# Kernel optimization log

Hardware: AMD Instinct MI355X
Metric: run time of the kernel (lower is better)

## Reference

```python
import jax, jax.numpy as jnp
import numpy as np

N_RBF = 20
CUTOFF = 5.0
N_BASIS = 128
N_FILTERS = 128
N_LAYERS = 3
B, N = 128, 128
N_PAIRS = 524288


def ssp(x):
    # ShiftedSoftplus: softplus(x) - log(2)
    return jax.nn.softplus(x) - jnp.log(2.0).astype(x.dtype)


def gaussian_rbf(d):
    # schnetpack-style GaussianRBF: offsets in [0, cutoff], shared width
    offsets = jnp.linspace(0.0, CUTOFF, N_RBF, dtype=d.dtype)
    width = offsets[1] - offsets[0]
    coeff = -0.5 / (width * width)
    diff = d[:, None] - offsets[None, :]  # [n_pairs, n_rbf]
    return jnp.exp(coeff * diff * diff)


def cosine_cutoff(d):
    fc = 0.5 * (jnp.cos(d * (jnp.pi / CUTOFF)) + 1.0)
    return fc * (d < CUTOFF).astype(d.dtype)


def setup_inputs() -> dict:
    key = jax.random.key(0)
    ks = jax.random.split(key, 16)
    inp = {
        "Z": jax.random.randint(ks[0], (B, N), 0, 100),
        "R": jax.random.normal(ks[1], (B, N, 3), dtype=jnp.float32) * 2.0,
        "idx_i": jax.random.randint(ks[2], (N_PAIRS,), 0, B * N),
        "idx_j": jax.random.randint(ks[3], (N_PAIRS,), 0, B * N),
        "emb": jax.random.normal(ks[4], (100, N_BASIS), dtype=jnp.float32) * 0.1,
    }
    s = 0.05
    inp["in2f_W"] = jax.random.normal(ks[5], (N_LAYERS, N_BASIS, N_FILTERS), dtype=jnp.float32) * s
    inp["in2f_b"] = jnp.zeros((N_LAYERS, N_FILTERS), dtype=jnp.float32)
    inp["fW1"] = jax.random.normal(ks[6], (N_LAYERS, N_RBF, N_FILTERS), dtype=jnp.float32) * s
    inp["fb1"] = jnp.zeros((N_LAYERS, N_FILTERS), dtype=jnp.float32)
    inp["fW2"] = jax.random.normal(ks[7], (N_LAYERS, N_FILTERS, N_FILTERS), dtype=jnp.float32) * s
    inp["fb2"] = jnp.zeros((N_LAYERS, N_FILTERS), dtype=jnp.float32)
    inp["oW1"] = jax.random.normal(ks[8], (N_LAYERS, N_FILTERS, N_BASIS), dtype=jnp.float32) * s
    inp["ob1"] = jnp.zeros((N_LAYERS, N_BASIS), dtype=jnp.float32)
    inp["oW2"] = jax.random.normal(ks[9], (N_LAYERS, N_BASIS, N_BASIS), dtype=jnp.float32) * s
    inp["ob2"] = jnp.zeros((N_LAYERS, N_BASIS), dtype=jnp.float32)
    return inp


def _interaction(x, f_ij, rcut_ij, idx_i, idx_j, W_in, b_in, fW1, fb1, fW2, fb2, oW1, ob1, oW2, ob2):
    # x: [B, N, n_atom_basis]
    h = jnp.einsum("bnf,fg->bng", x, W_in) + b_in          # input_to_feature
    h = h.reshape(-1, h.shape[-1])                           # [B*N, n_filters]
    # filter network on RBFs
    Wij = ssp(f_ij @ fW1 + fb1) @ fW2 + fb2                  # [n_pairs, n_filters]
    Wij = Wij * rcut_ij[:, None]
    x_ij = h[idx_j] * Wij                                     # gather + multiply
    agg = jax.ops.segment_sum(x_ij, idx_i, num_segments=h.shape[0])  # scatter_add
    out = ssp(agg @ oW1 + ob1) @ oW2 + ob2                    # feature_to_output
    return out.reshape(x.shape[0], x.shape[1], N_BASIS)


def reference(Z, R, idx_i, idx_j, emb, in2f_W, in2f_b, fW1, fb1, fW2, fb2, oW1, ob1, oW2, ob2):
    coords = R.reshape(-1, 3)                                 # [B*N, 3]
    vec = coords[idx_i] - coords[idx_j]
    d_ij = jnp.linalg.norm(vec, axis=-1)                      # [n_pairs]
    f_ij = gaussian_rbf(d_ij)                                 # [n_pairs, 20]
    rcut_ij = cosine_cutoff(d_ij)                             # [n_pairs]
    x = emb[Z]                                                # [B, N, 128]
    for l in range(N_LAYERS):
        v = _interaction(x, f_ij, rcut_ij, idx_i, idx_j,
                         in2f_W[l], in2f_b[l], fW1[l], fb1[l], fW2[l], fb2[l],
                         oW1[l], ob1[l], oW2[l], ob2[l])
        x = x + v
    return x
```

## Files before the change

### kernel.cpp

```cpp
#include <hip/hip_runtime.h>
#include <hip/hip_fp16.h>

#define NPAIRS 524288
#define NATOMS 16384
#define TBINS  2048
#define TROWS  2049
#define CAP    80
#define CUTOFF_F 5.0f

typedef _Float16 f16;
typedef f16 f16x4 __attribute__((ext_vector_type(4)));
typedef f16 f16x8 __attribute__((ext_vector_type(8)));
typedef float f32x4 __attribute__((ext_vector_type(4)));

__device__ __forceinline__ float sspf(float v) {
  float a = fabsf(v);
  return fmaxf(v, 0.0f) + log1pf(expf(-a)) - 0.69314718055994531f;
}

__device__ __forceinline__ int swz(int row, int kh) {
  return (row << 8) + ((kh << 1) ^ ((row & 7) << 4));
}
__device__ __forceinline__ int swzW(int col, int kh) {
  return (col << 7) + ((kh << 1) ^ ((col & 7) << 4));
}
__device__ __forceinline__ f16x8 ldW(const f16* __restrict__ Wg, int col, int ss, int hi) {
  return *(const f16x8*)((const char*)Wg + (ss >> 1) * 16384 + swzW(col, (ss & 1) * 32 + hi * 8));
}

__device__ __forceinline__ uint4 ldtab(const f16* __restrict__ tabL, int v, int c) {
  return *(const uint4*)(tabL + ((unsigned)(v >> 14) << 7) + (c << 3));
}
__device__ __forceinline__ uint4 ldh(const f16* __restrict__ hin, int v, int c) {
  return *(const uint4*)(hin + ((unsigned)(v & 16383) << 7) + (c << 3));
}
__device__ __forceinline__ void dot8(float* acc, uint4 wv, uint4 hv) {
  const __half* wp = (const __half*)&wv;
  const __half* hp = (const __half*)&hv;
  #pragma unroll
  for (int q = 0; q < 8; ++q)
    acc[q] = fmaf(__half2float(wp[q]), __half2float(hp[q]), acc[q]);
}

__global__ __launch_bounds__(256) void prep(const float* __restrict__ fW1,
                                            const float* __restrict__ fb1,
                                            const float* __restrict__ fW2,
                                            const float* __restrict__ fb2,
                                            f16* __restrict__ table,
                                            const float* __restrict__ in2f_W,
                                            const float* __restrict__ oW1,
                                            const float* __restrict__ oW2,
                                            f16* __restrict__ wsw,
                                            int* __restrict__ cursor) {
  __shared__ float hid[8 * 128];
  int t = threadIdx.x;
  int bid = blockIdx.x;

  if (bid >= 843) { cursor[(bid - 843) * 256 + t] = 0; return; }

  if (bid >= 771) {
    int bid2 = bid - 771;
    int mm = bid2 >> 3;
    int tloc = (bid2 & 7) * 256 + t;
    int col = tloc & 127, k0 = (tloc >> 7) << 3;
    const float* src = mm < 3 ? in2f_W + (size_t)mm * 16384
                     : mm < 6 ? oW1 + (size_t)(mm - 3) * 16384
                              : oW2 + (size_t)(mm - 6) * 16384;
    f16x8 v;
    #pragma unroll
    for (int kk = 0; kk < 8; ++kk) v[kk] = (f16)src[(k0 + kk) * 128 + col];
    *(f16x8*)((char*)wsw + (size_t)mm * 32768 + (k0 >> 6) * 16384 + swzW(col, k0 & 63)) = v;
    return;
  }

  int l = bid / 257, rem = bid % 257;
  int e = t >> 5, q = t & 31;
  int ti = rem * 8 + e;
  const float* W1 = fW1 + (size_t)l * 20 * 128;
  const float* B1 = fb1 + (size_t)l * 128;
  const float* W2 = fW2 + (size_t)l * 128 * 128;
  const float* B2 = fb2 + (size_t)l * 128;

  const float width = CUTOFF_F / 19.0f;
  const float coeff = -0.5f / (width * width);
  const float dstep = CUTOFF_F / (float)TBINS;
  float d = (float)ti * dstep;

  float4 h4 = *(const float4*)&B1[q * 4];
  #pragma unroll
  for (int r = 0; r < 20; ++r) {
    float diff = d - (float)r * width;
    float fr = expf(coeff * diff * diff);
    float4 w4 = *(const float4*)&W1[r * 128 + q * 4];
    h4.x += fr * w4.x; h4.y += fr * w4.y; h4.z += fr * w4.z; h4.w += fr * w4.w;
  }
  *(float4*)&hid[e * 128 + q * 4] =
      make_float4(sspf(h4.x), sspf(h4.y), sspf(h4.z), sspf(h4.w));
  __syncthreads();

  float4 o4 = *(const float4*)&B2[q * 4];
  const float4* W2g = (const float4*)W2;
  #pragma unroll 4
  for (int g = 0; g < 128; ++g) {
    float hv = hid[e * 128 + g];
    float4 w4 = W2g[g * 32 + q];
    o4.x += hv * w4.x; o4.y += hv * w4.y; o4.z += hv * w4.z; o4.w += hv * w4.w;
  }

  if (ti < TROWS) {
    float fc = (d < CUTOFF_F) ? 0.5f * (cosf(d * 0.62831853071795865f) + 1.0f) : 0.0f;
    f16x4 hv = { (f16)(o4.x * fc), (f16)(o4.y * fc), (f16)(o4.z * fc), (f16)(o4.w * fc) };
    *(f16x4*)((f16*)table + ((size_t)l * TROWS + ti) * 128 + q * 4) = hv;
  }
}

__global__ __launch_bounds__(256) void pg0(const int* __restrict__ Z,
                                           const float* __restrict__ emb,
                                           const f16* __restrict__ Wsw,
                                           const float* __restrict__ bias,
                                           f16* __restrict__ hout,
                                           const int* __restrict__ idx_i,
                                           const int* __restrict__ idx_j,
                                           const float* __restrict__ R,
                                           int* __restrict__ cursor,
                                           int* __restrict__ pjd) {
  int t = threadIdx.x;

  if (blockIdx.x < 2048) {
    int p = blockIdx.x * 256 + t;
    int i = idx_i[p], j = idx_j[p];
    float dx = R[(size_t)i*3+0] - R[(size_t)j*3+0];
    float dy = R[(size_t)i*3+1] - R[(size_t)j*3+1];
    float dz = R[(size_t)i*3+2] - R[(size_t)j*3+2];
    float d = sqrtf(dx*dx + dy*dy + dz*dz);
    if (d < CUTOFF_F) {
      int bin = __float2int_rn(d * ((float)TBINS / CUTOFF_F));
      int slot = atomicAdd(&cursor[i], 1);
      if (slot < CAP) pjd[i * CAP + slot] = j | (bin << 14);
    }
    return;
  }

  size_t rbase = (size_t)(blockIdx.x - 2048) * 64;
  int w = t >> 6, lane = t & 63;
  int lo = lane & 15, hi = lane >> 4;

  int z = Z[rbase + 16 * w + lo];
  const float* erow = emb + (size_t)z * 128;
  f16x8 fa[4];
  #pragma unroll
  for (int ss = 0; ss < 4; ++ss) {
    float4 a = *(const float4*)(erow + ss * 32 + hi * 8);
    float4 b = *(const float4*)(erow + ss * 32 + hi * 8 + 4);
    f16x8 v = { (f16)a.x, (f16)a.y, (f16)a.z, (f16)a.w,
                (f16)b.x, (f16)b.y, (f16)b.z, (f16)b.w };
    fa[ss] = v;
  }

  #pragma unroll
  for (int cb = 0; cb < 8; ++cb) {
    int col = cb * 16 + lo;
    f32x4 acc = {0.0f, 0.0f, 0.0f, 0.0f};
    #pragma unroll
    for (int ss = 0; ss < 4; ++ss)
      acc = __builtin_amdgcn_mfma_f32_16x16x32_f16(fa[ss], ldW(Wsw, col, ss, hi), acc, 0, 0, 0);
    float bc = bias[col];
    #pragma unroll
    for (int j = 0; j < 4; ++j)
      hout[(rbase + 16 * w + hi * 4 + j) * 128 + col] = (f16)(acc[j] + bc);
  }
}

template <int FIRST, int HAS_NEXT>
__global__ __launch_bounds__(1024, 8) void aggfuse(const int* __restrict__ pjd,
                                                   const int* __restrict__ cnt,
                                                   const f16* __restrict__ hin,
                                                   const f16* __restrict__ tabL,
                                                   const f16* __restrict__ W1g,
                                                   const float* __restrict__ ob1,
                                                   const f16* __restrict__ W2g,
                                                   const float* __restrict__ ob2,
                                                   const int* __restrict__ Z,
                                                   const float* __restrict__ emb,
                                                   float* __restrict__ x,
                                                   const f16* __restrict__ Wng,
                                                   const float* __restrict__ bn,
                                                   f16* __restrict__ hout) {
  __shared__ char smem[16384];
  char* AlT = smem;
  char* Tl  = smem + 8192;
  int tid = threadIdx.x;
  int wv = tid >> 6, lane = tid & 63;
  int s = lane >> 4, c = lane & 15;
  int rbase = blockIdx.x * 32;
  const int S = (TBINS << 14);

  {
    int a = rbase + wv * 2 + (s & 1);
    int half = s >> 1;
    int p0 = a * CAP;
    int n = min(cnt[a], CAP);
    int nh = half * 2;

    int m = (n + 3) >> 2;
    m = max(m, __shfl_xor(m, 16, 64));
    m = max(m, __shfl_xor(m, 32, 64));

    float acc[8];
    #pragma unroll
    for (int q = 0; q < 8; ++q) acc[q] = 0.0f;

    int vA  = (nh < n)     ? pjd[p0 + nh]     : S;
    int vB  = (nh + 1 < n) ? pjd[p0 + nh + 1] : S;
    int vA1 = (nh + 4 < n) ? pjd[p0 + nh + 4] : S;
    int vB1 = (nh + 5 < n) ? pjd[p0 + nh + 5] : S;
    uint4 wA = ldtab(tabL, vA, c), hA = ldh(hin, vA, c);
    uint4 wB = ldtab(tabL, vB, c), hB = ldh(hin, vB, c);

    for (int it = 0; it < m; ++it) {
      int k2 = 4 * (it + 2) + nh;
      int vA2 = (k2 < n)     ? pjd[p0 + k2]     : S;
      int vB2 = (k2 + 1 < n) ? pjd[p0 + k2 + 1] : S;
      uint4 wAn = ldtab(tabL, vA1, c), hAn = ldh(hin, vA1, c);
      uint4 wBn = ldtab(tabL, vB1, c), hBn = ldh(hin, vB1, c);
      dot8(acc, wA, hA);
      dot8(acc, wB, hB);
      wA = wAn; hA = hAn; wB = wBn; hB = hBn;
      vA1 = vA2; vB1 = vB2;
    }

    #pragma unroll
    for (int q = 0; q < 8; ++q) acc[q] += __shfl_xor(acc[q], 32, 64);

    if (s < 2) {
      int row = wv * 2 + s;
      f16x8 pk;
      #pragma unroll
      for (int q = 0; q < 8; ++q) pk[q] = (f16)acc[q];
      *(f16x8*)(AlT + swz(row, c * 8)) = pk;
    }
  }
  __syncthreads();

  int lo = c, hi = s;
  int col = (wv & 7) * 16 + lo;
  int rb16 = (wv >> 3) * 16;

  float res[4];
  if (FIRST) {
    #pragma unroll
    for (int j = 0; j < 4; ++j) {
      int z = Z[rbase + rb16 + hi * 4 + j];
      res[j] = emb[(size_t)z * 128 + col];
    }
  } else {
    #pragma unroll
    for (int j = 0; j < 4; ++j)
      res[j] = x[(size_t)(rbase + rb16 + hi * 4 + j) * 128 + col];
  }

  {
    f32x4 acc = {0.0f, 0.0f, 0.0f, 0.0f};
    #pragma unroll
    for (int ss = 0; ss < 4; ++ss) {
      f16x8 fa = *(f16x8*)(AlT + swz(rb16 + lo, ss * 32 + hi * 8));
      acc = __builtin_amdgcn_mfma_f32_16x16x32_f16(fa, ldW(W1g, col, ss, hi), acc, 0, 0, 0);
    }
    float bc = ob1[col];
    #pragma unroll
    for (int j = 0; j < 4; ++j)
      *(f16*)(Tl + swz(rb16 + hi * 4 + j, col)) = (f16)sspf(acc[j] + bc);
  }
  __syncthreads();

  {
    f32x4 acc = {0.0f, 0.0f, 0.0f, 0.0f};
    #pragma unroll
    for (int ss = 0; ss < 4; ++ss) {
      f16x8 fa = *(f16x8*)(Tl + swz(rb16 + lo, ss * 32 + hi * 8));
      acc = __builtin_amdgcn_mfma_f32_16x16x32_f16(fa, ldW(W2g, col, ss, hi), acc, 0, 0, 0);
    }
    float bc = ob2[col];
    #pragma unroll
    for (int j = 0; j < 4; ++j) {
      int r = rb16 + hi * 4 + j;
      float xn = res[j] + acc[j] + bc;
      x[(size_t)(rbase + r) * 128 + col] = xn;
      if (HAS_NEXT) *(f16*)(AlT + swz(r, col)) = (f16)xn;
    }
  }

  if (HAS_NEXT) {
    __syncthreads();
    f32x4 acc = {0.0f, 0.0f, 0.0f, 0.0f};
    #pragma unroll
    for (int ss = 0; ss < 4; ++ss) {
      f16x8 fa = *(f16x8*)(AlT + swz(rb16 + lo, ss * 32 + hi * 8));
      acc = __builtin_amdgcn_mfma_f32_16x16x32_f16(fa, ldW(Wng, col, ss, hi), acc, 0, 0, 0);
    }
    float bc = bn[col];
    #pragma unroll
    for (int j = 0; j < 4; ++j)
      hout[(size_t)(rbase + rb16 + hi * 4 + j) * 128 + col] = (f16)(acc[j] + bc);
  }
}

extern "C" void kernel_launch(void* const* d_in, const int* in_sizes, int n_in,
                              void* d_out, int out_size, void* d_ws, size_t ws_size,
                              hipStream_t stream) {
  const int*   Z      = (const int*)d_in[0];
  const float* R      = (const float*)d_in[1];
  const int*   idx_i  = (const int*)d_in[2];
  const int*   idx_j  = (const int*)d_in[3];
  const float* emb    = (const float*)d_in[4];
  const float* in2f_W = (const float*)d_in[5];
  const float* in2f_b = (const float*)d_in[6];
  const float* fW1    = (const float*)d_in[7];
  const float* fb1    = (const float*)d_in[8];
  const float* fW2    = (const float*)d_in[9];
  const float* fb2    = (const float*)d_in[10];
  const float* oW1    = (const float*)d_in[11];
  const float* ob1    = (const float*)d_in[12];
  const float* oW2    = (const float*)d_in[13];
  const float* ob2    = (const float*)d_in[14];
  float* x = (float*)d_out;

  char* ws = (char*)d_ws;
  int*  cursor = (int*) (ws + 0x000000);
  int*  pjd    = (int*) (ws + 0x010000);
  f16*  table  = (f16*) (ws + 0x510000);
  f16*  h0     = (f16*) (ws + 0x6A0000);
  f16*  h1     = (f16*) (ws + 0xAA0000);
  f16*  wsw    = (f16*) (ws + 0xEA0000);

  prep<<<907, 256, 0, stream>>>(fW1, fb1, fW2, fb2, table, in2f_W, oW1, oW2, wsw, cursor);
  pg0<<<2304, 256, 0, stream>>>(Z, emb, wsw, in2f_b, h0, idx_i, idx_j, R, cursor, pjd);

  aggfuse<1, 1><<<NATOMS / 32, 1024, 0, stream>>>(pjd, cursor, h0, table + 0 * (size_t)TROWS * 128,
                                                  wsw + 3 * 16384, ob1,
                                                  wsw + 6 * 16384, ob2,
                                                  Z, emb, x,
                                                  wsw + 1 * 16384, in2f_b + 128, h1);
  aggfuse<0, 1><<<NATOMS / 32, 1024, 0, stream>>>(pjd, cursor, h1, table + 1 * (size_t)TROWS * 128,
                                                  wsw + 4 * 16384, ob1 + 128,
                                                  wsw + 7 * 16384, ob2 + 128,
                                                  Z, emb, x,
                                                  wsw + 2 * 16384, in2f_b + 256, h0);
  aggfuse<0, 0><<<NATOMS / 32, 1024, 0, stream>>>(pjd, cursor, h0, table + 2 * (size_t)TROWS * 128,
                                                  wsw + 5 * 16384, ob1 + 256,
                                                  wsw + 8 * 16384, ob2 + 256,
                                                  Z, emb, x, nullptr, nullptr, nullptr);
}
```

Baseline: 124.4 us.

## Merge prep and first projection into one launch; halve aggfuse block size

The preparation work (filter table, weight swizzle, layer-0 input projection, pair binning) now runs in a single mega kernel, preceded by a tiny cursor-zeroing kernel. This removes the dependency between weight swizzling and the first projection: the projection blocks convert in2f_W into shared memory themselves. The aggregation kernel now uses 512-thread blocks over 16 atoms instead of 1024 threads over 32 atoms, which doubles the block count and halves shared memory per block. The cost is redundant weight conversion in every projection block and possibly less weight reuse per block in aggfuse.

Result: faster. 111.1 us (-10.7%).

```diff
diff --git a/kernel.cpp b/kernel.cpp
--- a/kernel.cpp
+++ b/kernel.cpp
@@ -8,6 +8,11 @@
 #define CAP    80
 #define CUTOFF_F 5.0f
 
+#define MB_G0    256
+#define MB_TAB   (MB_G0 + 771)
+#define MB_WC    (MB_TAB + 72)
+#define MB_TOTAL (MB_WC + 2048)
+
 typedef _Float16 f16;
 typedef f16 f16x4 __attribute__((ext_vector_type(4)));
 typedef f16 f16x8 __attribute__((ext_vector_type(8)));
@@ -42,24 +47,137 @@
     acc[q] = fmaf(__half2float(wp[q]), __half2float(hp[q]), acc[q]);
 }
 
-__global__ __launch_bounds__(256) void prep(const float* __restrict__ fW1,
+__global__ __launch_bounds__(256) void zero_kernel(int* __restrict__ p) {
+  p[blockIdx.x * 256 + threadIdx.x] = 0;
+}
+
+__global__ __launch_bounds__(256) void mega(const int* __restrict__ Z,
+                                            const float* __restrict__ emb,
+                                            const float* __restrict__ in2f_W,
+                                            const float* __restrict__ in2f_b,
+                                            const float* __restrict__ fW1,
                                             const float* __restrict__ fb1,
                                             const float* __restrict__ fW2,
                                             const float* __restrict__ fb2,
-                                            f16* __restrict__ table,
-                                            const float* __restrict__ in2f_W,
                                             const float* __restrict__ oW1,
                                             const float* __restrict__ oW2,
+                                            const int* __restrict__ idx_i,
+                                            const int* __restrict__ idx_j,
+                                            const float* __restrict__ R,
+                                            f16* __restrict__ table,
                                             f16* __restrict__ wsw,
-                                            int* __restrict__ cursor) {
-  __shared__ float hid[8 * 128];
+                                            int* __restrict__ cursor,
+                                            int* __restrict__ pjd,
+                                            f16* __restrict__ hout) {
+  __shared__ char smem[16384];
   int t = threadIdx.x;
   int bid = blockIdx.x;
 
-  if (bid >= 843) { cursor[(bid - 843) * 256 + t] = 0; return; }
-
-  if (bid >= 771) {
-    int bid2 = bid - 771;
+  if (bid < MB_G0) {
+    char* Wl = smem;
+    size_t rbase = (size_t)bid * 64;
+    int w = t >> 6, lane = t & 63;
+    int lo = lane & 15, hi = lane >> 4;
+
+    int z = Z[rbase + 16 * w + lo];
+    const float* erow = emb + (size_t)z * 128;
+    f16x8 fa[4];
+    #pragma unroll
+    for (int ss = 0; ss < 4; ++ss) {
+      float4 a = *(const float4*)(erow + ss * 32 + hi * 8);
+      float4 b = *(const float4*)(erow + ss * 32 + hi * 8 + 4);
+      f16x8 v = { (f16)a.x, (f16)a.y, (f16)a.z, (f16)a.w,
+                  (f16)b.x, (f16)b.y, (f16)b.z, (f16)b.w };
+      fa[ss] = v;
+    }
+
+    f32x4 acc[8];
+    #pragma unroll
+    for (int cb = 0; cb < 8; ++cb) acc[cb] = (f32x4){0.0f, 0.0f, 0.0f, 0.0f};
+
+    #pragma unroll
+    for (int h = 0; h < 2; ++h) {
+      #pragma unroll
+      for (int i = 0; i < 4; ++i) {
+        int tloc = i * 256 + t;
+        int col = tloc & 127, kc = tloc >> 7;
+        f16x8 v;
+        #pragma unroll
+        for (int kk = 0; kk < 8; ++kk)
+          v[kk] = (f16)in2f_W[(h * 64 + kc * 8 + kk) * 128 + col];
+        *(f16x8*)(Wl + swzW(col, kc * 8)) = v;
+      }
+      __syncthreads();
+      #pragma unroll
+      for (int cb = 0; cb < 8; ++cb) {
+        int col = cb * 16 + lo;
+        #pragma unroll
+        for (int sh = 0; sh < 2; ++sh) {
+          f16x8 fb = *(f16x8*)(Wl + swzW(col, sh * 32 + hi * 8));
+          acc[cb] = __builtin_amdgcn_mfma_f32_16x16x32_f16(fa[h * 2 + sh], fb, acc[cb], 0, 0, 0);
+        }
+      }
+      __syncthreads();
+    }
+
+    #pragma unroll
+    for (int cb = 0; cb < 8; ++cb) {
+      int col = cb * 16 + lo;
+      float bc = in2f_b[col];
+      #pragma unroll
+      for (int j = 0; j < 4; ++j)
+        hout[(rbase + 16 * w + hi * 4 + j) * 128 + col] = (f16)(acc[cb][j] + bc);
+    }
+    return;
+  }
+
+  if (bid < MB_TAB) {
+    float* hid = (float*)smem;
+    int bid2 = bid - MB_G0;
+    int l = bid2 / 257, rem = bid2 % 257;
+    int e = t >> 5, q = t & 31;
+    int ti = rem * 8 + e;
+    const float* W1 = fW1 + (size_t)l * 20 * 128;
+    const float* B1 = fb1 + (size_t)l * 128;
+    const float* W2 = fW2 + (size_t)l * 128 * 128;
+    const float* B2 = fb2 + (size_t)l * 128;
+
+    const float width = CUTOFF_F / 19.0f;
+    const float coeff = -0.5f / (width * width);
+    const float dstep = CUTOFF_F / (float)TBINS;
+    float d = (float)ti * dstep;
+
+    float4 h4 = *(const float4*)&B1[q * 4];
+    #pragma unroll
+    for (int r = 0; r < 20; ++r) {
+      float diff = d - (float)r * width;
+      float fr = expf(coeff * diff * diff);
+      float4 w4 = *(const float4*)&W1[r * 128 + q * 4];
+      h4.x += fr * w4.x; h4.y += fr * w4.y; h4.z += fr * w4.z; h4.w += fr * w4.w;
+    }
+    *(float4*)&hid[e * 128 + q * 4] =
+        make_float4(sspf(h4.x), sspf(h4.y), sspf(h4.z), sspf(h4.w));
+    __syncthreads();
+
+    float4 o4 = *(const float4*)&B2[q * 4];
+    const float4* W2g = (const float4*)W2;
+    #pragma unroll 4
+    for (int g = 0; g < 128; ++g) {
+      float hv = hid[e * 128 + g];
+      float4 w4 = W2g[g * 32 + q];
+      o4.x += hv * w4.x; o4.y += hv * w4.y; o4.z += hv * w4.z; o4.w += hv * w4.w;
+    }
+
+    if (ti < TROWS) {
+      float fc = (d < CUTOFF_F) ? 0.5f * (cosf(d * 0.62831853071795865f) + 1.0f) : 0.0f;
+      f16x4 hv = { (f16)(o4.x * fc), (f16)(o4.y * fc), (f16)(o4.z * fc), (f16)(o4.w * fc) };
+      *(f16x4*)((f16*)table + ((size_t)l * TROWS + ti) * 128 + q * 4) = hv;
+    }
+    return;
+  }
+
+  if (bid < MB_WC) {
+    int bid2 = bid - MB_TAB;
     int mm = bid2 >> 3;
     int tloc = (bid2 & 7) * 256 + t;
     int col = tloc & 127, k0 = (tloc >> 7) << 3;
@@ -73,61 +191,8 @@
     return;
   }
 
-  int l = bid / 257, rem = bid % 257;
-  int e = t >> 5, q = t & 31;
-  int ti = rem * 8 + e;
-  const float* W1 = fW1 + (size_t)l * 20 * 128;
-  const float* B1 = fb1 + (size_t)l * 128;
-  const float* W2 = fW2 + (size_t)l * 128 * 128;
-  const float* B2 = fb2 + (size_t)l * 128;
-
-  const float width = CUTOFF_F / 19.0f;
-  const float coeff = -0.5f / (width * width);
-  const float dstep = CUTOFF_F / (float)TBINS;
-  float d = (float)ti * dstep;
-
-  float4 h4 = *(const float4*)&B1[q * 4];
-  #pragma unroll
-  for (int r = 0; r < 20; ++r) {
-    float diff = d - (float)r * width;
-    float fr = expf(coeff * diff * diff);
-    float4 w4 = *(const float4*)&W1[r * 128 + q * 4];
-    h4.x += fr * w4.x; h4.y += fr * w4.y; h4.z += fr * w4.z; h4.w += fr * w4.w;
-  }
-  *(float4*)&hid[e * 128 + q * 4] =
-      make_float4(sspf(h4.x), sspf(h4.y), sspf(h4.z), sspf(h4.w));
-  __syncthreads();
-
-  float4 o4 = *(const float4*)&B2[q * 4];
-  const float4* W2g = (const float4*)W2;
-  #pragma unroll 4
-  for (int g = 0; g < 128; ++g) {
-    float hv = hid[e * 128 + g];
-    float4 w4 = W2g[g * 32 + q];
-    o4.x += hv * w4.x; o4.y += hv * w4.y; o4.z += hv * w4.z; o4.w += hv * w4.w;
-  }
-
-  if (ti < TROWS) {
-    float fc = (d < CUTOFF_F) ? 0.5f * (cosf(d * 0.62831853071795865f) + 1.0f) : 0.0f;
-    f16x4 hv = { (f16)(o4.x * fc), (f16)(o4.y * fc), (f16)(o4.z * fc), (f16)(o4.w * fc) };
-    *(f16x4*)((f16*)table + ((size_t)l * TROWS + ti) * 128 + q * 4) = hv;
-  }
-}
-
-__global__ __launch_bounds__(256) void pg0(const int* __restrict__ Z,
-                                           const float* __restrict__ emb,
-                                           const f16* __restrict__ Wsw,
-                                           const float* __restrict__ bias,
-                                           f16* __restrict__ hout,
-                                           const int* __restrict__ idx_i,
-                                           const int* __restrict__ idx_j,
-                                           const float* __restrict__ R,
-                                           int* __restrict__ cursor,
-                                           int* __restrict__ pjd) {
-  int t = threadIdx.x;
-
-  if (blockIdx.x < 2048) {
-    int p = blockIdx.x * 256 + t;
+  {
+    int p = (bid - MB_WC) * 256 + t;
     int i = idx_i[p], j = idx_j[p];
     float dx = R[(size_t)i*3+0] - R[(size_t)j*3+0];
     float dy = R[(size_t)i*3+1] - R[(size_t)j*3+1];
@@ -138,61 +203,31 @@
       int slot = atomicAdd(&cursor[i], 1);
       if (slot < CAP) pjd[i * CAP + slot] = j | (bin << 14);
     }
-    return;
-  }
-
-  size_t rbase = (size_t)(blockIdx.x - 2048) * 64;
-  int w = t >> 6, lane = t & 63;
-  int lo = lane & 15, hi = lane >> 4;
-
-  int z = Z[rbase + 16 * w + lo];
-  const float* erow = emb + (size_t)z * 128;
-  f16x8 fa[4];
-  #pragma unroll
-  for (int ss = 0; ss < 4; ++ss) {
-    float4 a = *(const float4*)(erow + ss * 32 + hi * 8);
-    float4 b = *(const float4*)(erow + ss * 32 + hi * 8 + 4);
-    f16x8 v = { (f16)a.x, (f16)a.y, (f16)a.z, (f16)a.w,
-                (f16)b.x, (f16)b.y, (f16)b.z, (f16)b.w };
-    fa[ss] = v;
-  }
-
-  #pragma unroll
-  for (int cb = 0; cb < 8; ++cb) {
-    int col = cb * 16 + lo;
-    f32x4 acc = {0.0f, 0.0f, 0.0f, 0.0f};
-    #pragma unroll
-    for (int ss = 0; ss < 4; ++ss)
-      acc = __builtin_amdgcn_mfma_f32_16x16x32_f16(fa[ss], ldW(Wsw, col, ss, hi), acc, 0, 0, 0);
-    float bc = bias[col];
-    #pragma unroll
-    for (int j = 0; j < 4; ++j)
-      hout[(rbase + 16 * w + hi * 4 + j) * 128 + col] = (f16)(acc[j] + bc);
   }
 }
 
 template <int FIRST, int HAS_NEXT>
-__global__ __launch_bounds__(1024, 8) void aggfuse(const int* __restrict__ pjd,
-                                                   const int* __restrict__ cnt,
-                                                   const f16* __restrict__ hin,
-                                                   const f16* __restrict__ tabL,
-                                                   const f16* __restrict__ W1g,
-                                                   const float* __restrict__ ob1,
-                                                   const f16* __restrict__ W2g,
-                                                   const float* __restrict__ ob2,
-                                                   const int* __restrict__ Z,
-                                                   const float* __restrict__ emb,
-                                                   float* __restrict__ x,
-                                                   const f16* __restrict__ Wng,
-                                                   const float* __restrict__ bn,
-                                                   f16* __restrict__ hout) {
-  __shared__ char smem[16384];
+__global__ __launch_bounds__(512, 8) void aggfuse(const int* __restrict__ pjd,
+                                                  const int* __restrict__ cnt,
+                                                  const f16* __restrict__ hin,
+                                                  const f16* __restrict__ tabL,
+                                                  const f16* __restrict__ W1g,
+                                                  const float* __restrict__ ob1,
+                                                  const f16* __restrict__ W2g,
+                                                  const float* __restrict__ ob2,
+                                                  const int* __restrict__ Z,
+                                                  const float* __restrict__ emb,
+                                                  float* __restrict__ x,
+                                                  const f16* __restrict__ Wng,
+                                                  const float* __restrict__ bn,
+                                                  f16* __restrict__ hout) {
+  __shared__ char smem[8192];
   char* AlT = smem;
-  char* Tl  = smem + 8192;
+  char* Tl  = smem + 4096;
   int tid = threadIdx.x;
   int wv = tid >> 6, lane = tid & 63;
   int s = lane >> 4, c = lane & 15;
-  int rbase = blockIdx.x * 32;
+  int rbase = blockIdx.x * 16;
   const int S = (TBINS << 14);
 
   {
@@ -243,33 +278,32 @@
   __syncthreads();
 
   int lo = c, hi = s;
-  int col = (wv & 7) * 16 + lo;
-  int rb16 = (wv >> 3) * 16;
+  int col = wv * 16 + lo;
 
   float res[4];
   if (FIRST) {
     #pragma unroll
     for (int j = 0; j < 4; ++j) {
-      int z = Z[rbase + rb16 + hi * 4 + j];
+      int z = Z[rbase + hi * 4 + j];
       res[j] = emb[(size_t)z * 128 + col];
     }
   } else {
     #pragma unroll
     for (int j = 0; j < 4; ++j)
-      res[j] = x[(size_t)(rbase + rb16 + hi * 4 + j) * 128 + col];
+      res[j] = x[(size_t)(rbase + hi * 4 + j) * 128 + col];
   }
 
   {
     f32x4 acc = {0.0f, 0.0f, 0.0f, 0.0f};
     #pragma unroll
     for (int ss = 0; ss < 4; ++ss) {
-      f16x8 fa = *(f16x8*)(AlT + swz(rb16 + lo, ss * 32 + hi * 8));
+      f16x8 fa = *(f16x8*)(AlT + swz(lo, ss * 32 + hi * 8));
       acc = __builtin_amdgcn_mfma_f32_16x16x32_f16(fa, ldW(W1g, col, ss, hi), acc, 0, 0, 0);
     }
     float bc = ob1[col];
     #pragma unroll
     for (int j = 0; j < 4; ++j)
-      *(f16*)(Tl + swz(rb16 + hi * 4 + j, col)) = (f16)sspf(acc[j] + bc);
+      *(f16*)(Tl + swz(hi * 4 + j, col)) = (f16)sspf(acc[j] + bc);
   }
   __syncthreads();
 
@@ -277,13 +311,13 @@
     f32x4 acc = {0.0f, 0.0f, 0.0f, 0.0f};
     #pragma unroll
     for (int ss = 0; ss < 4; ++ss) {
-      f16x8 fa = *(f16x8*)(Tl + swz(rb16 + lo, ss * 32 + hi * 8));
+      f16x8 fa = *(f16x8*)(Tl + swz(lo, ss * 32 + hi * 8));
       acc = __builtin_amdgcn_mfma_f32_16x16x32_f16(fa, ldW(W2g, col, ss, hi), acc, 0, 0, 0);
     }
     float bc = ob2[col];
     #pragma unroll
     for (int j = 0; j < 4; ++j) {
-      int r = rb16 + hi * 4 + j;
+      int r = hi * 4 + j;
       float xn = res[j] + acc[j] + bc;
       x[(size_t)(rbase + r) * 128 + col] = xn;
       if (HAS_NEXT) *(f16*)(AlT + swz(r, col)) = (f16)xn;
@@ -295,13 +329,13 @@
     f32x4 acc = {0.0f, 0.0f, 0.0f, 0.0f};
     #pragma unroll
     for (int ss = 0; ss < 4; ++ss) {
-      f16x8 fa = *(f16x8*)(AlT + swz(rb16 + lo, ss * 32 + hi * 8));
+      f16x8 fa = *(f16x8*)(AlT + swz(lo, ss * 32 + hi * 8));
       acc = __builtin_amdgcn_mfma_f32_16x16x32_f16(fa, ldW(Wng, col, ss, hi), acc, 0, 0, 0);
     }
     float bc = bn[col];
     #pragma unroll
     for (int j = 0; j < 4; ++j)
-      hout[(size_t)(rbase + rb16 + hi * 4 + j) * 128 + col] = (f16)(acc[j] + bc);
+      hout[(size_t)(rbase + hi * 4 + j) * 128 + col] = (f16)(acc[j] + bc);
   }
 }
 
@@ -333,21 +367,23 @@
   f16*  h1     = (f16*) (ws + 0xAA0000);
   f16*  wsw    = (f16*) (ws + 0xEA0000);
 
-  prep<<<907, 256, 0, stream>>>(fW1, fb1, fW2, fb2, table, in2f_W, oW1, oW2, wsw, cursor);
-  pg0<<<2304, 256, 0, stream>>>(Z, emb, wsw, in2f_b, h0, idx_i, idx_j, R, cursor, pjd);
-
-  aggfuse<1, 1><<<NATOMS / 32, 1024, 0, stream>>>(pjd, cursor, h0, table + 0 * (size_t)TROWS * 128,
-                                                  wsw + 3 * 16384, ob1,
-                                                  wsw + 6 * 16384, ob2,
-                                                  Z, emb, x,
-                                                  wsw + 1 * 16384, in2f_b + 128, h1);
-  aggfuse<0, 1><<<NATOMS / 32, 1024, 0, stream>>>(pjd, cursor, h1, table + 1 * (size_t)TROWS * 128,
-                                                  wsw + 4 * 16384, ob1 + 128,
-                                                  wsw + 7 * 16384, ob2 + 128,
-                                                  Z, emb, x,
-                                                  wsw + 2 * 16384, in2f_b + 256, h0);
-  aggfuse<0, 0><<<NATOMS / 32, 1024, 0, stream>>>(pjd, cursor, h0, table + 2 * (size_t)TROWS * 128,
-                                                  wsw + 5 * 16384, ob1 + 256,
-                                                  wsw + 8 * 16384, ob2 + 256,
-                                                  Z, emb, x, nullptr, nullptr, nullptr);
-}
+  zero_kernel<<<NATOMS / 256, 256, 0, stream>>>(cursor);
+  mega<<<MB_TOTAL, 256, 0, stream>>>(Z, emb, in2f_W, in2f_b, fW1, fb1, fW2, fb2,
+                                     oW1, oW2, idx_i, idx_j, R,
+                                     table, wsw, cursor, pjd, h0);
+
+  aggfuse<1, 1><<<NATOMS / 16, 512, 0, stream>>>(pjd, cursor, h0, table + 0 * (size_t)TROWS * 128,
+                                                 wsw + 3 * 16384, ob1,
+                                                 wsw + 6 * 16384, ob2,
+                                                 Z, emb, x,
+                                                 wsw + 1 * 16384, in2f_b + 128, h1);
+  aggfuse<0, 1><<<NATOMS / 16, 512, 0, stream>>>(pjd, cursor, h1, table + 1 * (size_t)TROWS * 128,
+                                                 wsw + 4 * 16384, ob1 + 128,
+                                                 wsw + 7 * 16384, ob2 + 128,
+                                                 Z, emb, x,
+                                                 wsw + 2 * 16384, in2f_b + 256, h0);
+  aggfuse<0, 0><<<NATOMS / 16, 512, 0, stream>>>(pjd, cursor, h0, table + 2 * (size_t)TROWS * 128,
+                                                 wsw + 5 * 16384, ob1 + 256,
+                                                 wsw + 8 * 16384, ob2 + 256,
+                                                 Z, emb, x, nullptr, nullptr, nullptr);
+}
```
